# Optimization experiments

Measured on AMD Instinct MI355X. Metric: run time of the kernel, lower is better.

The kernel has to match this reference:

```python
import jax, jax.numpy as jnp
import numpy as np

TEMPERATURE = 0.5
EPS = 1e-8  # matches torch cosine_similarity eps guard semantics (norm clamp)


def setup_inputs() -> dict:
    key = jax.random.key(0)
    k1, k2 = jax.random.split(key)
    B, D = 4096, 256
    z_i = jax.random.normal(k1, (B, D), dtype=jnp.float32)
    z_j = jax.random.normal(k2, (B, D), dtype=jnp.float32)
    return {"z_i": z_i, "z_j": z_j}


def reference(z_i, z_j):
    B = z_i.shape[0]
    z = jnp.concatenate([z_i, z_j], axis=0)            # [2B, D]
    # cosine similarity: normalize once, then GEMM
    norm = jnp.maximum(jnp.linalg.norm(z, axis=1, keepdims=True), EPS)
    zn = z / norm                                       # [2B, D]
    sim = zn @ zn.T                                     # [2B, 2B]
    # positives: diag(sim, +B) and diag(sim, -B)
    idx = jnp.arange(B)
    sim_ij = sim[idx, idx + B]
    sim_ji = sim[idx + B, idx]
    positives = jnp.concatenate([sim_ij, sim_ji])       # [2B]
    # masked denominator: exclude self-similarity
    mask = 1.0 - jnp.eye(2 * B, dtype=sim.dtype)
    denom = jnp.sum(mask * jnp.exp(sim / TEMPERATURE), axis=1)  # [2B]
    all_losses = -jnp.log(jnp.exp(positives / TEMPERATURE) / denom)
    return jnp.sum(all_losses) / (2 * B)
```

## Files before the change

### kernel.cpp

```cpp
#include <hip/hip_runtime.h>
#include <hip/hip_bf16.h>
#include <cstdint>
#include <cstddef>
#include <math.h>

#define D 256
#define TEMP_INV 2.0f
#define EPS_NORM 1e-8f
#define NTILES 2080

typedef __attribute__((ext_vector_type(8))) short bf16x8;
typedef __attribute__((ext_vector_type(4))) float f32x4;

__global__ void __launch_bounds__(256) normalize_rows(
    const float* __restrict__ zi, const float* __restrict__ zj,
    __hip_bfloat16* __restrict__ zn, float* __restrict__ out, int B) {
  const int wid = threadIdx.x >> 6;
  const int lane = threadIdx.x & 63;
  if (blockIdx.x == 0 && threadIdx.x == 0) out[0] = 0.0f;
#pragma unroll
  for (int it = 0; it < 4; ++it) {
    int row = it * 2048 + blockIdx.x * 4 + wid;
    const float* src = (row < B) ? (zi + (size_t)row * D)
                                 : (zj + (size_t)(row - B) * D);
    float4 v = ((const float4*)src)[lane];
    float ss = v.x * v.x + v.y * v.y + v.z * v.z + v.w * v.w;
    for (int off = 32; off; off >>= 1) ss += __shfl_xor(ss, off);
    float rn = 1.0f / fmaxf(sqrtf(ss), EPS_NORM);
    union { ushort4 u; __hip_bfloat16 h[4]; } o;
    o.h[0] = __float2bfloat16(v.x * rn);
    o.h[1] = __float2bfloat16(v.y * rn);
    o.h[2] = __float2bfloat16(v.z * rn);
    o.h[3] = __float2bfloat16(v.w * rn);
    ((ushort4*)zn)[(size_t)row * (D / 4) + lane] = o.u;
  }
}

__device__ __forceinline__ void decode_tile(int t, int Nb, int& by, int& bx) {
  float fb = (2.0f * Nb + 1.0f -
              sqrtf((float)((2 * Nb + 1) * (2 * Nb + 1) - 8 * t))) * 0.5f;
  int y = (int)fb;
  while ((y + 1) * Nb - ((y + 1) * y) / 2 <= t) ++y;
  while (y * Nb - (y * (y - 1)) / 2 > t) --y;
  by = y;
  bx = y + (t - (y * Nb - (y * (y - 1)) / 2));
}

__global__ void __launch_bounds__(256, 4) ntxent_gemm(
    const __hip_bfloat16* __restrict__ zn,
    float* __restrict__ part, float* __restrict__ pos, int B) {
  __shared__ __align__(16) __hip_bfloat16 Ash[128 * 64];
  __shared__ __align__(16) __hip_bfloat16 Bsh[128 * 64];

  const int N = 2 * B;
  const int Nb = N / 128;
  int by, bx;
  decode_tile(blockIdx.x, Nb, by, bx);
  const int bm = by * 128;
  const int bn = bx * 128;
  const bool isDiag = (by == bx);
  const bool isPos = (bx == by + B / 128);

  const int tid = threadIdx.x;
  const int wid = tid >> 6;
  const int lane = tid & 63;
  const int wy = wid >> 1, wx = wid & 1;
  const int wrow0 = wid * 32;

  const int lr = lane >> 3;
  const int c8 = lane & 7;

  const int frow = lane & 15;
  const int quad = lane >> 4;
  const int f7 = frow & 7;

  f32x4 acc[4][4] = {};

  const __hip_bfloat16* gA = zn + (size_t)(bm + wrow0 + lr) * D + c8 * 8;
  const __hip_bfloat16* gB = zn + (size_t)(bn + wrow0 + lr) * D + c8 * 8;
  const int ldsoff = (wrow0 + lr) * 64 + (c8 ^ lr) * 8;

  float4 va0 = *(const float4*)(gA + 0 * 8 * D);
  float4 va1 = *(const float4*)(gA + 1 * 8 * D);
  float4 va2 = *(const float4*)(gA + 2 * 8 * D);
  float4 va3 = *(const float4*)(gA + 3 * 8 * D);
  float4 vb0 = *(const float4*)(gB + 0 * 8 * D);
  float4 vb1 = *(const float4*)(gB + 1 * 8 * D);
  float4 vb2 = *(const float4*)(gB + 2 * 8 * D);
  float4 vb3 = *(const float4*)(gB + 3 * 8 * D);

#pragma unroll
  for (int k0i = 0; k0i < 4; ++k0i) {
    __syncthreads();
    *(float4*)&Ash[ldsoff + 0 * 8 * 64] = va0;
    *(float4*)&Ash[ldsoff + 1 * 8 * 64] = va1;
    *(float4*)&Ash[ldsoff + 2 * 8 * 64] = va2;
    *(float4*)&Ash[ldsoff + 3 * 8 * 64] = va3;
    *(float4*)&Bsh[ldsoff + 0 * 8 * 64] = vb0;
    *(float4*)&Bsh[ldsoff + 1 * 8 * 64] = vb1;
    *(float4*)&Bsh[ldsoff + 2 * 8 * 64] = vb2;
    *(float4*)&Bsh[ldsoff + 3 * 8 * 64] = vb3;
    __syncthreads();
    if (k0i < 3) {
      const int k0 = (k0i + 1) * 64;
      va0 = *(const float4*)(gA + 0 * 8 * D + k0);
      va1 = *(const float4*)(gA + 1 * 8 * D + k0);
      va2 = *(const float4*)(gA + 2 * 8 * D + k0);
      va3 = *(const float4*)(gA + 3 * 8 * D + k0);
      vb0 = *(const float4*)(gB + 0 * 8 * D + k0);
      vb1 = *(const float4*)(gB + 1 * 8 * D + k0);
      vb2 = *(const float4*)(gB + 2 * 8 * D + k0);
      vb3 = *(const float4*)(gB + 3 * 8 * D + k0);
    }
#pragma unroll
    for (int kk = 0; kk < 2; ++kk) {
      bf16x8 a[4], b[4];
#pragma unroll
      for (int i = 0; i < 4; ++i)
        a[i] = *(const bf16x8*)
            &Ash[(wy * 64 + i * 16 + frow) * 64 + ((kk * 4 + quad) ^ f7) * 8];
#pragma unroll
      for (int j = 0; j < 4; ++j)
        b[j] = *(const bf16x8*)
            &Bsh[(wx * 64 + j * 16 + frow) * 64 + ((kk * 4 + quad) ^ f7) * 8];
#pragma unroll
      for (int i = 0; i < 4; ++i)
#pragma unroll
        for (int j = 0; j < 4; ++j)
          acc[i][j] =
              __builtin_amdgcn_mfma_f32_16x16x32_bf16(a[i], b[j], acc[i][j], 0, 0, 0);
    }
  }

  __syncthreads();
  float* red = (float*)Ash;

  const int colq = lane & 15;
  float cs[4] = {0.0f, 0.0f, 0.0f, 0.0f};
#pragma unroll
  for (int i = 0; i < 4; ++i) {
#pragma unroll
    for (int r = 0; r < 4; ++r) {
      int rowloc = wy * 64 + i * 16 + quad * 4 + r;
      int row = bm + rowloc;
      float rs = 0.0f;
#pragma unroll
      for (int j = 0; j < 4; ++j) {
        int col = bn + wx * 64 + j * 16 + colq;
        float v = acc[i][j][r];
        float e = __expf(v * TEMP_INV);
        e = (isDiag && col == row) ? 0.0f : e;
        rs += e;
        cs[j] += e;
        if (isPos && col == row + B) { pos[row] = v; pos[col] = v; }
      }
      rs += __shfl_xor(rs, 1);
      rs += __shfl_xor(rs, 2);
      rs += __shfl_xor(rs, 4);
      rs += __shfl_xor(rs, 8);
      if (colq == 0) red[rowloc * 2 + wx] = rs;
    }
  }
#pragma unroll
  for (int j = 0; j < 4; ++j) {
    float c = cs[j];
    c += __shfl_xor(c, 16);
    c += __shfl_xor(c, 32);
    if (quad == 0) red[256 + (wx * 64 + j * 16 + colq) * 2 + wy] = c;
  }
  __syncthreads();
  if (tid < 128) {
    part[(size_t)bx * N + bm + tid] = red[tid * 2] + red[tid * 2 + 1];
  } else if (!isDiag) {
    int t = tid - 128;
    part[(size_t)by * N + bn + t] = red[256 + t * 2] + red[256 + t * 2 + 1];
  }
}

__global__ void __launch_bounds__(256) finalize(
    const float* __restrict__ part, const float* __restrict__ pos,
    float* __restrict__ out, int N) {
  const int idx = blockIdx.x * 256 + threadIdx.x;
  const int NS = N / 128;
  float s = 0.0f;
#pragma unroll 8
  for (int k = 0; k < NS; ++k) s += part[(size_t)k * N + idx];
  float loss = __logf(s) - pos[idx] * TEMP_INV;
  for (int off = 32; off; off >>= 1) loss += __shfl_xor(loss, off);
  __shared__ float redsh[4];
  if ((threadIdx.x & 63) == 0) redsh[threadIdx.x >> 6] = loss;
  __syncthreads();
  if (threadIdx.x == 0) {
    float t = redsh[0] + redsh[1] + redsh[2] + redsh[3];
    atomicAdd(out, t / (float)N);
  }
}

extern "C" void kernel_launch(void* const* d_in, const int* in_sizes, int n_in,
                              void* d_out, int out_size, void* d_ws, size_t ws_size,
                              hipStream_t stream) {
  const float* zi = (const float*)d_in[0];
  const float* zj = (const float*)d_in[1];
  const int B = in_sizes[0] / D;
  const int N = 2 * B;

  __hip_bfloat16* zn = (__hip_bfloat16*)d_ws;
  float* pos = (float*)((char*)d_ws + (size_t)N * D * sizeof(__hip_bfloat16));
  float* part = pos + N;

  normalize_rows<<<512, 256, 0, stream>>>(zi, zj, zn, (float*)d_out, B);
  ntxent_gemm<<<NTILES, 256, 0, stream>>>(zn, part, pos, B);
  finalize<<<N / 256, 256, 0, stream>>>(part, pos, (float*)d_out, N);
}
```

Measured before the change: 99.00 us.

## Use direct global-to-LDS loads with double-buffered shared tiles in GEMM

```diff
diff --git a/kernel.cpp b/kernel.cpp
--- a/kernel.cpp
+++ b/kernel.cpp
@@ -11,6 +11,11 @@
 
 typedef __attribute__((ext_vector_type(8))) short bf16x8;
 typedef __attribute__((ext_vector_type(4))) float f32x4;
+
+#define GLOAD16(g, l)                                                   \
+  __builtin_amdgcn_global_load_lds(                                     \
+      (const __attribute__((address_space(1))) void*)(g),               \
+      (__attribute__((address_space(3))) void*)(l), 16, 0, 0)
 
 __global__ void __launch_bounds__(256) normalize_rows(
     const float* __restrict__ zi, const float* __restrict__ zj,
@@ -46,11 +51,11 @@
   bx = y + (t - (y * Nb - (y * (y - 1)) / 2));
 }
 
-__global__ void __launch_bounds__(256, 4) ntxent_gemm(
+__global__ void __launch_bounds__(256, 2) ntxent_gemm(
     const __hip_bfloat16* __restrict__ zn,
     float* __restrict__ part, float* __restrict__ pos, int B) {
-  __shared__ __align__(16) __hip_bfloat16 Ash[128 * 64];
-  __shared__ __align__(16) __hip_bfloat16 Bsh[128 * 64];
+  __shared__ __align__(16) __hip_bfloat16 Ash[2][128 * 64];
+  __shared__ __align__(16) __hip_bfloat16 Bsh[2][128 * 64];
 
   const int N = 2 * B;
   const int Nb = N / 128;
@@ -76,41 +81,28 @@
 
   f32x4 acc[4][4] = {};
 
-  const __hip_bfloat16* gA = zn + (size_t)(bm + wrow0 + lr) * D + c8 * 8;
-  const __hip_bfloat16* gB = zn + (size_t)(bn + wrow0 + lr) * D + c8 * 8;
-  const int ldsoff = (wrow0 + lr) * 64 + (c8 ^ lr) * 8;
-
-  float4 va0 = *(const float4*)(gA + 0 * 8 * D);
-  float4 va1 = *(const float4*)(gA + 1 * 8 * D);
-  float4 va2 = *(const float4*)(gA + 2 * 8 * D);
-  float4 va3 = *(const float4*)(gA + 3 * 8 * D);
-  float4 vb0 = *(const float4*)(gB + 0 * 8 * D);
-  float4 vb1 = *(const float4*)(gB + 1 * 8 * D);
-  float4 vb2 = *(const float4*)(gB + 2 * 8 * D);
-  float4 vb3 = *(const float4*)(gB + 3 * 8 * D);
+  const __hip_bfloat16* gA =
+      zn + (size_t)(bm + wrow0 + lr) * D + (c8 ^ lr) * 8;
+  const __hip_bfloat16* gB =
+      zn + (size_t)(bn + wrow0 + lr) * D + (c8 ^ lr) * 8;
+
+#pragma unroll
+  for (int s = 0; s < 4; ++s) {
+    GLOAD16(gA + s * 8 * D, &Ash[0][(wrow0 + s * 8) * 64]);
+    GLOAD16(gB + s * 8 * D, &Bsh[0][(wrow0 + s * 8) * 64]);
+  }
+  __syncthreads();
 
 #pragma unroll
   for (int k0i = 0; k0i < 4; ++k0i) {
-    __syncthreads();
-    *(float4*)&Ash[ldsoff + 0 * 8 * 64] = va0;
-    *(float4*)&Ash[ldsoff + 1 * 8 * 64] = va1;
-    *(float4*)&Ash[ldsoff + 2 * 8 * 64] = va2;
-    *(float4*)&Ash[ldsoff + 3 * 8 * 64] = va3;
-    *(float4*)&Bsh[ldsoff + 0 * 8 * 64] = vb0;
-    *(float4*)&Bsh[ldsoff + 1 * 8 * 64] = vb1;
-    *(float4*)&Bsh[ldsoff + 2 * 8 * 64] = vb2;
-    *(float4*)&Bsh[ldsoff + 3 * 8 * 64] = vb3;
-    __syncthreads();
+    const int cur = k0i & 1;
     if (k0i < 3) {
       const int k0 = (k0i + 1) * 64;
-      va0 = *(const float4*)(gA + 0 * 8 * D + k0);
-      va1 = *(const float4*)(gA + 1 * 8 * D + k0);
-      va2 = *(const float4*)(gA + 2 * 8 * D + k0);
-      va3 = *(const float4*)(gA + 3 * 8 * D + k0);
-      vb0 = *(const float4*)(gB + 0 * 8 * D + k0);
-      vb1 = *(const float4*)(gB + 1 * 8 * D + k0);
-      vb2 = *(const float4*)(gB + 2 * 8 * D + k0);
-      vb3 = *(const float4*)(gB + 3 * 8 * D + k0);
+#pragma unroll
+      for (int s = 0; s < 4; ++s) {
+        GLOAD16(gA + s * 8 * D + k0, &Ash[cur ^ 1][(wrow0 + s * 8) * 64]);
+        GLOAD16(gB + s * 8 * D + k0, &Bsh[cur ^ 1][(wrow0 + s * 8) * 64]);
+      }
     }
 #pragma unroll
     for (int kk = 0; kk < 2; ++kk) {
@@ -118,11 +110,11 @@
 #pragma unroll
       for (int i = 0; i < 4; ++i)
         a[i] = *(const bf16x8*)
-            &Ash[(wy * 64 + i * 16 + frow) * 64 + ((kk * 4 + quad) ^ f7) * 8];
+            &Ash[cur][(wy * 64 + i * 16 + frow) * 64 + ((kk * 4 + quad) ^ f7) * 8];
 #pragma unroll
       for (int j = 0; j < 4; ++j)
         b[j] = *(const bf16x8*)
-            &Bsh[(wx * 64 + j * 16 + frow) * 64 + ((kk * 4 + quad) ^ f7) * 8];
+            &Bsh[cur][(wx * 64 + j * 16 + frow) * 64 + ((kk * 4 + quad) ^ f7) * 8];
 #pragma unroll
       for (int i = 0; i < 4; ++i)
 #pragma unroll
@@ -130,10 +122,10 @@
           acc[i][j] =
               __builtin_amdgcn_mfma_f32_16x16x32_bf16(a[i], b[j], acc[i][j], 0, 0, 0);
     }
-  }
-
-  __syncthreads();
-  float* red = (float*)Ash;
+    __syncthreads();
+  }
+
+  float* red = (float*)&Ash[0][0];
 
   const int colq = lane & 15;
   float cs[4] = {0.0f, 0.0f, 0.0f, 0.0f};
```

Result: slower. 115.5 us (+16.7%).
